# Optimization experiments

Measured on AMD Instinct MI355X. Metric: run time of the kernel, lower is better.

The kernel has to match this reference:

```python
import math
import jax, jax.numpy as jnp
import numpy as np

T = 2048       # sequence_length
H = 2048       # hidden_size
NH = 32        # num_attention_heads
NKV = 8        # num_key_value_heads
HD = 64        # head_dim
SW = 128       # sliding_window
QM = NH // NKV # q_mult (GQA group size)
ROPE_THETA = 10000.0
EPS = 1e-5


def setup_inputs() -> dict:
    key = jax.random.key(0)
    k_x, k_s, k_qkv, k_out = jax.random.split(key, 4)
    x = jax.random.normal(k_x, (T, H), dtype=jnp.float32)
    scale = jnp.ones((H,), dtype=jnp.float32)
    sinks = jax.random.normal(k_s, (NH,), dtype=jnp.float32) * 0.02
    qkv_dim = HD * (NH + 2 * NKV)  # 3072
    qkv_kernel = jax.random.normal(k_qkv, (H, qkv_dim), dtype=jnp.float32) * (1.0 / math.sqrt(H))
    qkv_bias = jnp.zeros((qkv_dim,), dtype=jnp.float32)
    out_kernel = jax.random.normal(k_out, (H, H), dtype=jnp.float32) * (1.0 / math.sqrt(H))
    out_bias = jnp.zeros((H,), dtype=jnp.float32)
    # RoPE tables: [T, HD//2]
    half = HD // 2
    inv_freq = 1.0 / (ROPE_THETA ** (np.arange(half, dtype=np.float64) / half))
    ang = np.outer(np.arange(T, dtype=np.float64), inv_freq)
    cos_table = jnp.asarray(np.cos(ang), dtype=jnp.float32)
    sin_table = jnp.asarray(np.sin(ang), dtype=jnp.float32)
    # causal + sliding-window additive mask [T, T]
    qp = np.arange(T, dtype=np.int32)[:, None]
    kp = np.arange(T, dtype=np.int32)[None, :]
    m = np.where(kp > qp, -np.inf, 0.0) + np.where(qp - kp > SW, -np.inf, 0.0)
    mask = jnp.asarray(m, dtype=jnp.float32)
    return dict(x=x, scale=scale, sinks=sinks, qkv_kernel=qkv_kernel,
                qkv_bias=qkv_bias, out_kernel=out_kernel, out_bias=out_bias,
                cos_table=cos_table, sin_table=sin_table, mask=mask)


def _rmsnorm(x, scale):
    t = x.astype(jnp.float32)
    rms = jnp.sqrt(jnp.mean(t * t, axis=-1, keepdims=True) + EPS)
    return ((t / rms) * scale).astype(x.dtype)


def _rope(x, cos, sin):
    # x: [T, ..., HD]; split-half rotation as in the reference RotaryEmbedding
    shp = x.shape
    xr = x.reshape(shp[0], -1, HD)
    c = cos[:, None, :].astype(xr.dtype)
    s = sin[:, None, :].astype(xr.dtype)
    x1, x2 = jnp.split(xr, 2, axis=-1)
    y = jnp.concatenate([x1 * c - x2 * s, x2 * c + x1 * s], axis=-1)
    return y.reshape(shp)


def reference(x, scale, sinks, qkv_kernel, qkv_bias, out_kernel, out_bias,
              cos_table, sin_table, mask):
    normed = _rmsnorm(x, scale)
    qkv = normed @ qkv_kernel + qkv_bias                 # [T, 3072]
    q_end = NH * HD
    k_end = q_end + NKV * HD
    q = qkv[:, :q_end].reshape(T, NKV, QM, HD)           # [T, nkv, qm, hd]
    k = qkv[:, q_end:k_end].reshape(T, NKV, HD)          # [T, nkv, hd]
    v = qkv[:, k_end:].reshape(T, NKV, HD)               # [T, nkv, hd]
    q = _rope(q, cos_table, sin_table)
    k = _rope(k, cos_table, sin_table)
    sm_scale = 1.0 / math.sqrt(float(HD))
    # GQA attention without materializing repeated K/V
    logits = jnp.einsum('qnmd,knd->nmqk', q, k) * sm_scale  # [nkv, qm, T, T]
    logits = logits + mask[None, None, :, :]
    sink_col = jnp.broadcast_to(sinks.reshape(NKV, QM, 1, 1), (NKV, QM, T, 1))
    logits = jnp.concatenate([logits, sink_col], axis=-1)   # [nkv, qm, T, T+1]
    weights = jax.nn.softmax(logits, axis=-1)[..., :-1]     # drop sink column
    attn = jnp.einsum('nmqk,knd->qnmd', weights, v).reshape(T, NH * HD)
    projected = attn @ out_kernel + out_bias
    return x + projected
```

## Files before the change

### kernel.cpp

```cpp
#include <hip/hip_runtime.h>
#include <hip/hip_bf16.h>
#include <stdint.h>

typedef __bf16 bf16_t;
typedef __attribute__((ext_vector_type(8))) __bf16 bf16x8;
typedef __attribute__((ext_vector_type(4))) __bf16 bf16x4;
typedef __attribute__((ext_vector_type(4))) float f32x4;

static constexpr int T_SEQ = 2048;
static constexpr int HID   = 2048;
static constexpr int NHEAD = 32;
static constexpr int NKVH  = 8;
static constexpr int HDIM  = 64;
static constexpr int QKVD  = 3072;

__device__ inline f32x4 mfma16(bf16x8 a, bf16x8 b, f32x4 c) {
    return __builtin_amdgcn_mfma_f32_16x16x32_bf16(a, b, c, 0, 0, 0);
}

__device__ inline void load_lds16(const bf16_t* g, bf16_t* l) {
    __builtin_amdgcn_global_load_lds(
        (const __attribute__((address_space(1))) void*)g,
        (__attribute__((address_space(3))) void*)l, 16, 0, 0);
}

__global__ __launch_bounds__(256) void prep_kernel(const float* __restrict__ Wq,
                                                   const float* __restrict__ Wo,
                                                   bf16_t* __restrict__ Tq,
                                                   bf16_t* __restrict__ To,
                                                   const float* __restrict__ x,
                                                   const float* __restrict__ scale,
                                                   bf16_t* __restrict__ normed) {
    __shared__ float tile[64 * 65];
    int b = blockIdx.x;
    const int t = threadIdx.x;
    if (b < 2560) {
        const float* in; bf16_t* out; int NN, KK, bx, by;
        if (b < 1536) { in = Wq; out = Tq; NN = QKVD; KK = HID; bx = b % 48; by = b / 48; }
        else { b -= 1536; in = Wo; out = To; NN = HID; KK = HID; bx = b % 32; by = b / 32; }
        const int c4 = (t & 15) * 4;
#pragma unroll
        for (int i = 0; i < 4; ++i) {
            int r = (t >> 4) + i * 16;
            float4 v = *(const float4*)(in + (size_t)(by*64 + r) * NN + bx*64 + c4);
            tile[r*65 + c4 + 0] = v.x; tile[r*65 + c4 + 1] = v.y;
            tile[r*65 + c4 + 2] = v.z; tile[r*65 + c4 + 3] = v.w;
        }
        __syncthreads();
        const int kc = t & 7;
#pragma unroll
        for (int i = 0; i < 2; ++i) {
            int n = (t >> 3) + i * 32;
            bf16x8 o;
#pragma unroll
            for (int j = 0; j < 8; ++j) o[j] = (bf16_t)tile[(kc*8 + j)*65 + n];
            *(bf16x8*)(out + (size_t)(bx*64 + n) * KK + by*64 + kc*8) = o;
        }
    } else {
        int row = b - 2560;
        const float4* x4 = (const float4*)(x + (size_t)row * HID);
        const float4* s4 = (const float4*)scale;
        float4 v0 = x4[t], v1 = x4[t + 256];
        float ss = v0.x*v0.x + v0.y*v0.y + v0.z*v0.z + v0.w*v0.w
                 + v1.x*v1.x + v1.y*v1.y + v1.z*v1.z + v1.w*v1.w;
#pragma unroll
        for (int off = 32; off > 0; off >>= 1) ss += __shfl_down(ss, off);
        if ((t & 63) == 0) tile[t >> 6] = ss;
        __syncthreads();
        float total = tile[0] + tile[1] + tile[2] + tile[3];
        float inv = rsqrtf(total * (1.0f / HID) + 1e-5f);
        float4 sc0 = s4[t], sc1 = s4[t + 256];
        bf16_t* outr = normed + (size_t)row * HID;
        bf16x4 o0, o1;
        o0.x = (bf16_t)(v0.x*inv*sc0.x); o0.y = (bf16_t)(v0.y*inv*sc0.y);
        o0.z = (bf16_t)(v0.z*inv*sc0.z); o0.w = (bf16_t)(v0.w*inv*sc0.w);
        o1.x = (bf16_t)(v1.x*inv*sc1.x); o1.y = (bf16_t)(v1.y*inv*sc1.y);
        o1.z = (bf16_t)(v1.z*inv*sc1.z); o1.w = (bf16_t)(v1.w*inv*sc1.w);
        *(bf16x4*)(outr + 4*t)        = o0;
        *(bf16x4*)(outr + 1024 + 4*t) = o1;
    }
}

__global__ __launch_bounds__(256) void gemm_splitk(const bf16_t* __restrict__ A,
                                                   const bf16_t* __restrict__ Bt,
                                                   bf16_t* __restrict__ Cpart,
                                                   int M, int N, int K) {
    __shared__ __align__(16) bf16_t Asm[64 * 32];
    __shared__ __align__(16) bf16_t Bsm[128 * 32];
    const int tid = threadIdx.x;
    const int bm = blockIdx.y * 64, bn = blockIdx.x * 128;
    const int kh = K >> 1;
    const int kb = blockIdx.z * kh;
    const int lane = tid & 63, wave = tid >> 6;
    const int wm = (wave & 1) * 32, wn = (wave >> 1) * 64;
    const int lm = lane & 15, quad = lane >> 4;

    f32x4 acc[2][4];
#pragma unroll
    for (int i = 0; i < 2; ++i)
#pragma unroll
        for (int j = 0; j < 4; ++j) acc[i][j] = (f32x4){0.f, 0.f, 0.f, 0.f};

    const int cidA = wave * 64 + lane;
    const int rA = cidA >> 2, cA = (cidA & 3) ^ ((rA >> 1) & 3);
    const int cid0 = wave * 64 + lane;
    const int cid1 = cid0 + 256;
    const int r0 = cid0 >> 2, c0 = (cid0 & 3) ^ ((r0 >> 1) & 3);
    const int r1 = cid1 >> 2, c1 = (cid1 & 3) ^ ((r1 >> 1) & 3);
    const bf16_t* Ab = A  + (size_t)bm * K + kb;
    const bf16_t* Bb = Bt + (size_t)bn * K + kb;
    const size_t gaA = (size_t)rA * K + cA * 8;
    const size_t ga0 = (size_t)r0 * K + c0 * 8;
    const size_t ga1 = (size_t)r1 * K + c1 * 8;
    bf16_t* ldsA  = &Asm[wave * 512];
    bf16_t* ldsB0 = &Bsm[wave * 512];
    bf16_t* ldsB1 = &Bsm[2048 + wave * 512];

    const int swz = (quad ^ ((lm >> 1) & 3)) * 8;

    for (int k0 = 0; k0 < kh; k0 += 32) {
        load_lds16(Ab + gaA + k0, ldsA);
        load_lds16(Bb + ga0 + k0, ldsB0);
        load_lds16(Bb + ga1 + k0, ldsB1);
        __syncthreads();
        bf16x8 af[2], bfr[4];
#pragma unroll
        for (int i = 0; i < 2; ++i)
            af[i]  = *(const bf16x8*)&Asm[(wm + i*16 + lm)*32 + swz];
#pragma unroll
        for (int j = 0; j < 4; ++j)
            bfr[j] = *(const bf16x8*)&Bsm[(wn + j*16 + lm)*32 + swz];
#pragma unroll
        for (int i = 0; i < 2; ++i)
#pragma unroll
            for (int j = 0; j < 4; ++j) acc[i][j] = mfma16(af[i], bfr[j], acc[i][j]);
        __syncthreads();
    }

    bf16_t* Cp = Cpart + (size_t)blockIdx.z * M * N;
#pragma unroll
    for (int i = 0; i < 2; ++i) {
        int gr = bm + wm + i*16 + quad*4;
#pragma unroll
        for (int j = 0; j < 4; ++j) {
            int gc = bn + wn + j*16 + lm;
#pragma unroll
            for (int r = 0; r < 4; ++r)
                Cp[(size_t)(gr + r)*N + gc] = (bf16_t)acc[i][j][r];
        }
    }
}

__global__ __launch_bounds__(192) void rope_split(const bf16_t* __restrict__ qp0,
                                                  const bf16_t* __restrict__ qp1,
                                                  const float* __restrict__ qbias,
                                                  const float* __restrict__ cost,
                                                  const float* __restrict__ sint,
                                                  bf16_t* __restrict__ Qb,
                                                  bf16_t* __restrict__ Kb,
                                                  bf16_t* __restrict__ Vb) {
    const int t = blockIdx.x;
    const int hr = threadIdx.x >> 2, p0 = (threadIdx.x & 3) * 8;
    const bf16_t* r0 = qp0 + (size_t)t * QKVD + hr * 64;
    const bf16_t* r1 = qp1 + (size_t)t * QKVD + hr * 64;
    bf16x8 a1 = *(const bf16x8*)(r0 + p0);
    bf16x8 a2 = *(const bf16x8*)(r0 + p0 + 32);
    bf16x8 b1 = *(const bf16x8*)(r1 + p0);
    bf16x8 b2 = *(const bf16x8*)(r1 + p0 + 32);
    const float* qb = qbias + hr * 64;
    float x1[8], x2[8];
#pragma unroll
    for (int j = 0; j < 8; ++j) {
        x1[j] = (float)a1[j] + (float)b1[j] + qb[p0 + j];
        x2[j] = (float)a2[j] + (float)b2[j] + qb[p0 + j + 32];
    }
    bf16x8 w1, w2;
    if (hr < 40) {
        const float* c = cost + (size_t)t * 32 + p0;
        const float* s = sint + (size_t)t * 32 + p0;
#pragma unroll
        for (int j = 0; j < 8; ++j) {
            float cc = c[j], ss = s[j];
            w1[j] = (bf16_t)(x1[j]*cc - x2[j]*ss);
            w2[j] = (bf16_t)(x2[j]*cc + x1[j]*ss);
        }
    } else {
#pragma unroll
        for (int j = 0; j < 8; ++j) { w1[j] = (bf16_t)x1[j]; w2[j] = (bf16_t)x2[j]; }
    }
    bf16_t* dst;
    if (hr < 32)      dst = Qb + ((size_t)t*NHEAD + hr)      * HDIM;
    else if (hr < 40) dst = Kb + ((size_t)t*NKVH + (hr-32))  * HDIM;
    else              dst = Vb + ((size_t)t*NKVH + (hr-40))  * HDIM;
    *(bf16x8*)(dst + p0)      = w1;
    *(bf16x8*)(dst + p0 + 32) = w2;
}

__global__ __launch_bounds__(256) void combine_out(const bf16_t* __restrict__ p0,
                                                   const bf16_t* __restrict__ p1,
                                                   const float* __restrict__ bias,
                                                   const float* __restrict__ x,
                                                   float* __restrict__ out) {
    const int n4 = T_SEQ * HID / 4;
    for (int i4 = blockIdx.x * 256 + threadIdx.x; i4 < n4; i4 += gridDim.x * 256) {
        bf16x4 a = *(const bf16x4*)(p0 + (size_t)i4 * 4);
        bf16x4 b = *(const bf16x4*)(p1 + (size_t)i4 * 4);
        float4 xv = *(const float4*)(x + (size_t)i4 * 4);
        int col4 = (i4 * 4) & (HID - 1);
        float4 bi = *(const float4*)(bias + col4);
        float4 o;
        o.x = (float)a.x + (float)b.x + bi.x + xv.x;
        o.y = (float)a.y + (float)b.y + bi.y + xv.y;
        o.z = (float)a.z + (float)b.z + bi.z + xv.z;
        o.w = (float)a.w + (float)b.w + bi.w + xv.w;
        *(float4*)(out + (size_t)i4 * 4) = o;
    }
}

__global__ __launch_bounds__(256) void attn_kernel(const bf16_t* __restrict__ Qb,
                                                   const bf16_t* __restrict__ Kb,
                                                   const bf16_t* __restrict__ Vb,
                                                   const float* __restrict__ sinks,
                                                   bf16_t* __restrict__ attnb) {
    __shared__ __align__(16) bf16_t Vt[64 * 200];
    __shared__ __align__(16) bf16_t Ws[64 * 200];

    const int tid = threadIdx.x;
    const int qt = blockIdx.x, h = blockIdx.y;
    const int qs = qt * 64;
    const int nkv = h >> 2;

#pragma unroll
    for (int it = 0; it < 3; ++it) {
        int pu = tid + it * 256;
        int j = (pu >> 3) * 2, off = (pu & 7) * 8;
        int kg0 = qs - 128 + j; if (kg0 < 0) kg0 = 0;
        int kg1 = qs - 128 + j + 1; if (kg1 < 0) kg1 = 0;
        union { uint4 u; bf16_t e[8]; } v0, v1;
        v0.u = *(const uint4*)(Vb + ((size_t)kg0*NKVH + nkv)*HDIM + off);
        v1.u = *(const uint4*)(Vb + ((size_t)kg1*NKVH + nkv)*HDIM + off);
#pragma unroll
        for (int r = 0; r < 8; ++r) {
            union { uint u; bf16_t e[2]; } p;
            p.e[0] = v0.e[r]; p.e[1] = v1.e[r];
            *(uint*)&Vt[(off + r)*200 + j] = p.u;
        }
    }

    const int lane = tid & 63, wave = tid >> 6;
    const int lm = lane & 15, quad = lane >> 4;
    const int w16 = wave * 16;

    f32x4 S[12];
#pragma unroll
    for (int jt = 0; jt < 12; ++jt) S[jt] = (f32x4){0.f, 0.f, 0.f, 0.f};
    const bf16_t* Qrow = Qb + ((size_t)(qs + w16 + lm)*NHEAD + h)*HDIM + quad*8;
    int krow[12];
#pragma unroll
    for (int jt = 0; jt < 12; ++jt) {
        int kg = qs - 128 + jt*16 + lm;
        krow[jt] = kg < 0 ? 0 : kg;
    }
#pragma unroll
    for (int ks = 0; ks < 2; ++ks) {
        bf16x8 aq = *(const bf16x8*)(Qrow + ks*32);
#pragma unroll
        for (int jt = 0; jt < 12; ++jt) {
            bf16x8 bk = *(const bf16x8*)(Kb + ((size_t)krow[jt]*NKVH + nkv)*HDIM + ks*32 + quad*8);
            S[jt] = mfma16(aq, bk, S[jt]);
        }
    }

    const float sink = sinks[h];
#pragma unroll
    for (int reg = 0; reg < 4; ++reg) {
        const int qg = qs + w16 + quad*4 + reg;
        float mx = -1e30f;
#pragma unroll
        for (int jt = 0; jt < 12; ++jt) {
            int kg = qs - 128 + jt*16 + lm;
            float sv = S[jt][reg] * 0.125f;
            bool valid = (kg >= 0) && (kg <= qg) && (qg - kg <= 128);
            sv = valid ? sv : -1e30f;
            S[jt][reg] = sv;
            mx = fmaxf(mx, sv);
        }
#pragma unroll
        for (int off = 1; off < 16; off <<= 1) mx = fmaxf(mx, __shfl_xor(mx, off));
        float M = fmaxf(mx, sink);
        float sum = 0.f;
#pragma unroll
        for (int jt = 0; jt < 12; ++jt) {
            float e = __expf(S[jt][reg] - M);
            S[jt][reg] = e; sum += e;
        }
#pragma unroll
        for (int off = 1; off < 16; off <<= 1) sum += __shfl_xor(sum, off);
        float rden = 1.f / (sum + __expf(sink - M));
#pragma unroll
        for (int jt = 0; jt < 12; ++jt)
            Ws[(w16 + quad*4 + reg)*200 + jt*16 + lm] = (bf16_t)(S[jt][reg] * rden);
    }
    __syncthreads();

    f32x4 O[4];
#pragma unroll
    for (int nt = 0; nt < 4; ++nt) O[nt] = (f32x4){0.f, 0.f, 0.f, 0.f};
#pragma unroll
    for (int ks = 0; ks < 6; ++ks) {
        bf16x8 aw = *(const bf16x8*)&Ws[(w16 + lm)*200 + ks*32 + quad*8];
#pragma unroll
        for (int nt = 0; nt < 4; ++nt) {
            bf16x8 bv = *(const bf16x8*)&Vt[(nt*16 + lm)*200 + ks*32 + quad*8];
            O[nt] = mfma16(aw, bv, O[nt]);
        }
    }
#pragma unroll
    for (int nt = 0; nt < 4; ++nt)
#pragma unroll
        for (int reg = 0; reg < 4; ++reg)
            attnb[(size_t)(qs + w16 + quad*4 + reg)*HID + h*HDIM + nt*16 + lm] =
                (bf16_t)(O[nt][reg]);
}

extern "C" void kernel_launch(void* const* d_in, const int* in_sizes, int n_in,
                              void* d_out, int out_size, void* d_ws, size_t ws_size,
                              hipStream_t stream) {
    (void)in_sizes; (void)n_in; (void)out_size; (void)ws_size;
    const float* x          = (const float*)d_in[0];
    const float* scale      = (const float*)d_in[1];
    const float* sinks      = (const float*)d_in[2];
    const float* qkv_kernel = (const float*)d_in[3];
    const float* qkv_bias   = (const float*)d_in[4];
    const float* out_kernel = (const float*)d_in[5];
    const float* out_bias   = (const float*)d_in[6];
    const float* cos_t      = (const float*)d_in[7];
    const float* sin_t      = (const float*)d_in[8];
    float* out = (float*)d_out;

    char* ws = (char*)d_ws;
    const size_t MiB = 1048576;
    bf16_t* Wt_out = (bf16_t*)(ws);
    bf16_t* Wt_qkv = (bf16_t*)(ws + 8*MiB);
    bf16_t* attnb  = (bf16_t*)(ws + 8*MiB);
    bf16_t* normed = (bf16_t*)(ws + 20*MiB);
    bf16_t* qkvp   = (bf16_t*)(ws + 28*MiB);
    bf16_t* outp   = (bf16_t*)(ws + 28*MiB);
    bf16_t* Qb     = (bf16_t*)(ws + 52*MiB);
    bf16_t* Kb     = (bf16_t*)(ws + 60*MiB);
    bf16_t* Vb     = (bf16_t*)(ws + 62*MiB);

    prep_kernel<<<4608, 256, 0, stream>>>(qkv_kernel, out_kernel, Wt_qkv, Wt_out,
                                          x, scale, normed);
    gemm_splitk<<<dim3(QKVD/128, T_SEQ/64, 2), 256, 0, stream>>>(normed, Wt_qkv, qkvp,
                                                                 T_SEQ, QKVD, HID);
    rope_split<<<T_SEQ, 192, 0, stream>>>(qkvp, qkvp + (size_t)T_SEQ*QKVD, qkv_bias,
                                          cos_t, sin_t, Qb, Kb, Vb);
    attn_kernel<<<dim3(T_SEQ/64, NHEAD), 256, 0, stream>>>(Qb, Kb, Vb, sinks, attnb);
    gemm_splitk<<<dim3(HID/128, T_SEQ/64, 2), 256, 0, stream>>>(attnb, Wt_out, outp,
                                                                T_SEQ, HID, HID);
    combine_out<<<2048, 256, 0, stream>>>(outp, outp + (size_t)T_SEQ*HID, out_bias, x, out);
}
```

Baseline: 237.5 us.

## Enlarge GEMM tiles, fuse output reduction via atomics, drop combine kernel

Grows the split-K GEMM block tile from 64x128 to 128x128 and processes a K-step of 64 per barrier, raising MFMA work per LDS load and per synchronisation. The output projection now atomically adds both split-K halves in fp32 straight into the output, which the prep kernel pre-fills with x plus bias, so the combine kernel and its bf16 partial buffers go away. It also reorders the V transpose loads in attention for better coalescing. In exchange it uses more registers and LDS per block, launches fewer blocks, and adds atomic traffic and non-deterministic summation order.

New measurement: 231.2 us. 2.7% less time.

```diff
diff --git a/kernel.cpp b/kernel.cpp
--- a/kernel.cpp
+++ b/kernel.cpp
@@ -30,14 +30,16 @@
                                                    bf16_t* __restrict__ To,
                                                    const float* __restrict__ x,
                                                    const float* __restrict__ scale,
-                                                   bf16_t* __restrict__ normed) {
+                                                   bf16_t* __restrict__ normed,
+                                                   const float* __restrict__ obias,
+                                                   float* __restrict__ out) {
     __shared__ float tile[64 * 65];
     int b = blockIdx.x;
     const int t = threadIdx.x;
     if (b < 2560) {
-        const float* in; bf16_t* out; int NN, KK, bx, by;
-        if (b < 1536) { in = Wq; out = Tq; NN = QKVD; KK = HID; bx = b % 48; by = b / 48; }
-        else { b -= 1536; in = Wo; out = To; NN = HID; KK = HID; bx = b % 32; by = b / 32; }
+        const float* in; bf16_t* outw; int NN, KK, bx, by;
+        if (b < 1536) { in = Wq; outw = Tq; NN = QKVD; KK = HID; bx = b % 48; by = b / 48; }
+        else { b -= 1536; in = Wo; outw = To; NN = HID; KK = HID; bx = b % 32; by = b / 32; }
         const int c4 = (t & 15) * 4;
 #pragma unroll
         for (int i = 0; i < 4; ++i) {
@@ -54,12 +56,13 @@
             bf16x8 o;
 #pragma unroll
             for (int j = 0; j < 8; ++j) o[j] = (bf16_t)tile[(kc*8 + j)*65 + n];
-            *(bf16x8*)(out + (size_t)(bx*64 + n) * KK + by*64 + kc*8) = o;
+            *(bf16x8*)(outw + (size_t)(bx*64 + n) * KK + by*64 + kc*8) = o;
         }
     } else {
         int row = b - 2560;
         const float4* x4 = (const float4*)(x + (size_t)row * HID);
         const float4* s4 = (const float4*)scale;
+        const float4* b4 = (const float4*)obias;
         float4 v0 = x4[t], v1 = x4[t + 256];
         float ss = v0.x*v0.x + v0.y*v0.y + v0.z*v0.z + v0.w*v0.w
                  + v1.x*v1.x + v1.y*v1.y + v1.z*v1.z + v1.w*v1.w;
@@ -78,75 +81,105 @@
         o1.z = (bf16_t)(v1.z*inv*sc1.z); o1.w = (bf16_t)(v1.w*inv*sc1.w);
         *(bf16x4*)(outr + 4*t)        = o0;
         *(bf16x4*)(outr + 1024 + 4*t) = o1;
-    }
-}
-
+        float4 bb0 = b4[t], bb1 = b4[t + 256];
+        float4 oi0 = {v0.x + bb0.x, v0.y + bb0.y, v0.z + bb0.z, v0.w + bb0.w};
+        float4 oi1 = {v1.x + bb1.x, v1.y + bb1.y, v1.z + bb1.z, v1.w + bb1.w};
+        float* orow = out + (size_t)row * HID;
+        *(float4*)(orow + 4*t)        = oi0;
+        *(float4*)(orow + 1024 + 4*t) = oi1;
+    }
+}
+
+template <int ATOMIC>
 __global__ __launch_bounds__(256) void gemm_splitk(const bf16_t* __restrict__ A,
                                                    const bf16_t* __restrict__ Bt,
                                                    bf16_t* __restrict__ Cpart,
+                                                   float* __restrict__ Cred,
                                                    int M, int N, int K) {
-    __shared__ __align__(16) bf16_t Asm[64 * 32];
-    __shared__ __align__(16) bf16_t Bsm[128 * 32];
+    __shared__ __align__(16) bf16_t Asm[2 * 128 * 32];
+    __shared__ __align__(16) bf16_t Bsm[2 * 128 * 32];
     const int tid = threadIdx.x;
-    const int bm = blockIdx.y * 64, bn = blockIdx.x * 128;
+    const int bm = blockIdx.y * 128, bn = blockIdx.x * 128;
     const int kh = K >> 1;
     const int kb = blockIdx.z * kh;
     const int lane = tid & 63, wave = tid >> 6;
-    const int wm = (wave & 1) * 32, wn = (wave >> 1) * 64;
+    const int wm = (wave & 1) * 64, wn = (wave >> 1) * 64;
     const int lm = lane & 15, quad = lane >> 4;
 
-    f32x4 acc[2][4];
-#pragma unroll
-    for (int i = 0; i < 2; ++i)
+    f32x4 acc[4][4];
+#pragma unroll
+    for (int i = 0; i < 4; ++i)
 #pragma unroll
         for (int j = 0; j < 4; ++j) acc[i][j] = (f32x4){0.f, 0.f, 0.f, 0.f};
 
-    const int cidA = wave * 64 + lane;
-    const int rA = cidA >> 2, cA = (cidA & 3) ^ ((rA >> 1) & 3);
-    const int cid0 = wave * 64 + lane;
-    const int cid1 = cid0 + 256;
+    const int cid0 = tid, cid1 = tid + 256;
     const int r0 = cid0 >> 2, c0 = (cid0 & 3) ^ ((r0 >> 1) & 3);
     const int r1 = cid1 >> 2, c1 = (cid1 & 3) ^ ((r1 >> 1) & 3);
     const bf16_t* Ab = A  + (size_t)bm * K + kb;
     const bf16_t* Bb = Bt + (size_t)bn * K + kb;
-    const size_t gaA = (size_t)rA * K + cA * 8;
     const size_t ga0 = (size_t)r0 * K + c0 * 8;
     const size_t ga1 = (size_t)r1 * K + c1 * 8;
-    bf16_t* ldsA  = &Asm[wave * 512];
-    bf16_t* ldsB0 = &Bsm[wave * 512];
-    bf16_t* ldsB1 = &Bsm[2048 + wave * 512];
-
+    bf16_t* ldsA0a = &Asm[wave * 512];
+    bf16_t* ldsA0b = &Asm[2048 + wave * 512];
+    bf16_t* ldsA1a = &Asm[4096 + wave * 512];
+    bf16_t* ldsA1b = &Asm[4096 + 2048 + wave * 512];
+    bf16_t* ldsB0a = &Bsm[wave * 512];
+    bf16_t* ldsB0b = &Bsm[2048 + wave * 512];
+    bf16_t* ldsB1a = &Bsm[4096 + wave * 512];
+    bf16_t* ldsB1b = &Bsm[4096 + 2048 + wave * 512];
     const int swz = (quad ^ ((lm >> 1) & 3)) * 8;
 
-    for (int k0 = 0; k0 < kh; k0 += 32) {
-        load_lds16(Ab + gaA + k0, ldsA);
-        load_lds16(Bb + ga0 + k0, ldsB0);
-        load_lds16(Bb + ga1 + k0, ldsB1);
+    for (int k0 = 0; k0 < kh; k0 += 64) {
+        load_lds16(Ab + ga0 + k0,      ldsA0a);
+        load_lds16(Ab + ga1 + k0,      ldsA0b);
+        load_lds16(Ab + ga0 + k0 + 32, ldsA1a);
+        load_lds16(Ab + ga1 + k0 + 32, ldsA1b);
+        load_lds16(Bb + ga0 + k0,      ldsB0a);
+        load_lds16(Bb + ga1 + k0,      ldsB0b);
+        load_lds16(Bb + ga0 + k0 + 32, ldsB1a);
+        load_lds16(Bb + ga1 + k0 + 32, ldsB1b);
         __syncthreads();
-        bf16x8 af[2], bfr[4];
-#pragma unroll
-        for (int i = 0; i < 2; ++i)
-            af[i]  = *(const bf16x8*)&Asm[(wm + i*16 + lm)*32 + swz];
-#pragma unroll
-        for (int j = 0; j < 4; ++j)
-            bfr[j] = *(const bf16x8*)&Bsm[(wn + j*16 + lm)*32 + swz];
-#pragma unroll
-        for (int i = 0; i < 2; ++i)
-#pragma unroll
-            for (int j = 0; j < 4; ++j) acc[i][j] = mfma16(af[i], bfr[j], acc[i][j]);
+#pragma unroll
+        for (int ks = 0; ks < 2; ++ks) {
+            bf16x8 af[4], bfr[4];
+#pragma unroll
+            for (int i = 0; i < 4; ++i)
+                af[i]  = *(const bf16x8*)&Asm[ks*4096 + (wm + i*16 + lm)*32 + swz];
+#pragma unroll
+            for (int j = 0; j < 4; ++j)
+                bfr[j] = *(const bf16x8*)&Bsm[ks*4096 + (wn + j*16 + lm)*32 + swz];
+#pragma unroll
+            for (int i = 0; i < 4; ++i)
+#pragma unroll
+                for (int j = 0; j < 4; ++j) acc[i][j] = mfma16(af[i], bfr[j], acc[i][j]);
+        }
         __syncthreads();
     }
 
-    bf16_t* Cp = Cpart + (size_t)blockIdx.z * M * N;
-#pragma unroll
-    for (int i = 0; i < 2; ++i) {
-        int gr = bm + wm + i*16 + quad*4;
-#pragma unroll
-        for (int j = 0; j < 4; ++j) {
-            int gc = bn + wn + j*16 + lm;
-#pragma unroll
-            for (int r = 0; r < 4; ++r)
-                Cp[(size_t)(gr + r)*N + gc] = (bf16_t)acc[i][j][r];
+    if (ATOMIC) {
+#pragma unroll
+        for (int i = 0; i < 4; ++i) {
+            int gr = bm + wm + i*16 + quad*4;
+#pragma unroll
+            for (int j = 0; j < 4; ++j) {
+                int gc = bn + wn + j*16 + lm;
+#pragma unroll
+                for (int r = 0; r < 4; ++r)
+                    atomicAdd(&Cred[(size_t)(gr + r)*N + gc], acc[i][j][r]);
+            }
+        }
+    } else {
+        bf16_t* Cp = Cpart + (size_t)blockIdx.z * M * N;
+#pragma unroll
+        for (int i = 0; i < 4; ++i) {
+            int gr = bm + wm + i*16 + quad*4;
+#pragma unroll
+            for (int j = 0; j < 4; ++j) {
+                int gc = bn + wn + j*16 + lm;
+#pragma unroll
+                for (int r = 0; r < 4; ++r)
+                    Cp[(size_t)(gr + r)*N + gc] = (bf16_t)acc[i][j][r];
+            }
         }
     }
 }
@@ -196,27 +229,6 @@
     *(bf16x8*)(dst + p0 + 32) = w2;
 }
 
-__global__ __launch_bounds__(256) void combine_out(const bf16_t* __restrict__ p0,
-                                                   const bf16_t* __restrict__ p1,
-                                                   const float* __restrict__ bias,
-                                                   const float* __restrict__ x,
-                                                   float* __restrict__ out) {
-    const int n4 = T_SEQ * HID / 4;
-    for (int i4 = blockIdx.x * 256 + threadIdx.x; i4 < n4; i4 += gridDim.x * 256) {
-        bf16x4 a = *(const bf16x4*)(p0 + (size_t)i4 * 4);
-        bf16x4 b = *(const bf16x4*)(p1 + (size_t)i4 * 4);
-        float4 xv = *(const float4*)(x + (size_t)i4 * 4);
-        int col4 = (i4 * 4) & (HID - 1);
-        float4 bi = *(const float4*)(bias + col4);
-        float4 o;
-        o.x = (float)a.x + (float)b.x + bi.x + xv.x;
-        o.y = (float)a.y + (float)b.y + bi.y + xv.y;
-        o.z = (float)a.z + (float)b.z + bi.z + xv.z;
-        o.w = (float)a.w + (float)b.w + bi.w + xv.w;
-        *(float4*)(out + (size_t)i4 * 4) = o;
-    }
-}
-
 __global__ __launch_bounds__(256) void attn_kernel(const bf16_t* __restrict__ Qb,
                                                    const bf16_t* __restrict__ Kb,
                                                    const bf16_t* __restrict__ Vb,
@@ -230,20 +242,22 @@
     const int qs = qt * 64;
     const int nkv = h >> 2;
 
-#pragma unroll
-    for (int it = 0; it < 3; ++it) {
-        int pu = tid + it * 256;
-        int j = (pu >> 3) * 2, off = (pu & 7) * 8;
-        int kg0 = qs - 128 + j; if (kg0 < 0) kg0 = 0;
-        int kg1 = qs - 128 + j + 1; if (kg1 < 0) kg1 = 0;
-        union { uint4 u; bf16_t e[8]; } v0, v1;
-        v0.u = *(const uint4*)(Vb + ((size_t)kg0*NKVH + nkv)*HDIM + off);
-        v1.u = *(const uint4*)(Vb + ((size_t)kg1*NKVH + nkv)*HDIM + off);
-#pragma unroll
-        for (int r = 0; r < 8; ++r) {
-            union { uint u; bf16_t e[2]; } p;
-            p.e[0] = v0.e[r]; p.e[1] = v1.e[r];
-            *(uint*)&Vt[(off + r)*200 + j] = p.u;
+    {
+        const int off = (tid >> 5) * 8;
+#pragma unroll
+        for (int it = 0; it < 3; ++it) {
+            int j2 = (tid & 31) + 32 * it;
+            int kg0 = qs - 128 + 2*j2;     if (kg0 < 0) kg0 = 0;
+            int kg1 = qs - 128 + 2*j2 + 1; if (kg1 < 0) kg1 = 0;
+            union { uint4 u; bf16_t e[8]; } v0, v1;
+            v0.u = *(const uint4*)(Vb + ((size_t)kg0*NKVH + nkv)*HDIM + off);
+            v1.u = *(const uint4*)(Vb + ((size_t)kg1*NKVH + nkv)*HDIM + off);
+#pragma unroll
+            for (int r = 0; r < 8; ++r) {
+                union { uint u; bf16_t e[2]; } p;
+                p.e[0] = v0.e[r]; p.e[1] = v1.e[r];
+                *(uint*)&Vt[(off + r)*200 + 2*j2] = p.u;
+            }
         }
     }
 
@@ -345,19 +359,17 @@
     bf16_t* attnb  = (bf16_t*)(ws + 8*MiB);
     bf16_t* normed = (bf16_t*)(ws + 20*MiB);
     bf16_t* qkvp   = (bf16_t*)(ws + 28*MiB);
-    bf16_t* outp   = (bf16_t*)(ws + 28*MiB);
     bf16_t* Qb     = (bf16_t*)(ws + 52*MiB);
     bf16_t* Kb     = (bf16_t*)(ws + 60*MiB);
     bf16_t* Vb     = (bf16_t*)(ws + 62*MiB);
 
     prep_kernel<<<4608, 256, 0, stream>>>(qkv_kernel, out_kernel, Wt_qkv, Wt_out,
-                                          x, scale, normed);
-    gemm_splitk<<<dim3(QKVD/128, T_SEQ/64, 2), 256, 0, stream>>>(normed, Wt_qkv, qkvp,
-                                                                 T_SEQ, QKVD, HID);
+                                          x, scale, normed, out_bias, out);
+    gemm_splitk<0><<<dim3(QKVD/128, T_SEQ/128, 2), 256, 0, stream>>>(normed, Wt_qkv, qkvp,
+                                                                     nullptr, T_SEQ, QKVD, HID);
     rope_split<<<T_SEQ, 192, 0, stream>>>(qkvp, qkvp + (size_t)T_SEQ*QKVD, qkv_bias,
                                           cos_t, sin_t, Qb, Kb, Vb);
     attn_kernel<<<dim3(T_SEQ/64, NHEAD), 256, 0, stream>>>(Qb, Kb, Vb, sinks, attnb);
-    gemm_splitk<<<dim3(HID/128, T_SEQ/64, 2), 256, 0, stream>>>(attnb, Wt_out, outp,
-                                                                T_SEQ, HID, HID);
-    combine_out<<<2048, 256, 0, stream>>>(outp, outp + (size_t)T_SEQ*HID, out_bias, x, out);
-}
+    gemm_splitk<1><<<dim3(HID/128, T_SEQ/128, 2), 256, 0, stream>>>(attnb, Wt_out, nullptr,
+                                                                    out, T_SEQ, HID, HID);
+}
```
